# Performance work log

Hardware: AMD Instinct MI355X
Metric: run time of the kernel (lower is better)

## Reference

```python
import jax, jax.numpy as jnp
import numpy as np
from jax import lax

EPS_BN = 1e-5
SMOOTH = 1e-5


def conv3x3(x, w):
    # x: [N,C,H,W], w: [O,I,3,3], stride 1, padding 1 (SAME)
    return lax.conv_general_dilated(
        x, w, window_strides=(1, 1), padding='SAME',
        dimension_numbers=('NCHW', 'OIHW', 'NCHW'))


def batchnorm(x, gamma, beta):
    # training-mode BatchNorm2d: batch statistics over (N,H,W), biased var
    mean = jnp.mean(x, axis=(0, 2, 3), keepdims=True)
    var = jnp.mean(jnp.square(x - mean), axis=(0, 2, 3), keepdims=True)
    g = gamma.reshape(1, -1, 1, 1)
    b = beta.reshape(1, -1, 1, 1)
    return (x - mean) * lax.rsqrt(var + EPS_BN) * g + b


def tanimoto(a, b, axes):
    tpl = jnp.sum(a * b, axis=axes, keepdims=True)
    sq = jnp.sum(a * a + b * b, axis=axes, keepdims=True)
    return (tpl + SMOOTH) / (sq - tpl + SMOOTH)


def tanimoto_compl(a, b, axes):
    return 0.5 * (tanimoto(a, b, axes) + tanimoto(1.0 - a, 1.0 - b, axes))


def setup_inputs() -> dict:
    key = jax.random.key(0)
    ks = jax.random.split(key, 5)
    N, Cin, Cout, H, W = 8, 64, 64, 256, 256
    x = jax.random.normal(ks[0], (N, Cin, H, W), dtype=jnp.float32)
    fan = Cin * 9
    wq = jax.random.normal(ks[1], (Cout, Cin, 3, 3), dtype=jnp.float32) / np.sqrt(fan)
    wk = jax.random.normal(ks[2], (Cout, Cin, 3, 3), dtype=jnp.float32) / np.sqrt(fan)
    wv = jax.random.normal(ks[3], (Cout, Cin, 3, 3), dtype=jnp.float32) / np.sqrt(fan)
    ones = jnp.ones((Cout,), dtype=jnp.float32)
    zeros = jnp.zeros((Cout,), dtype=jnp.float32)
    return {
        'x': x,
        'wq': wq, 'gq': ones, 'bq': zeros,
        'wk': wk, 'gk': ones, 'bk': zeros,
        'wv': wv, 'gv': ones, 'bv': zeros,
        'g_norm': ones, 'b_norm': zeros,
    }


def reference(x, wq, gq, bq, wk, gk, bk, wv, gv, bv, g_norm, b_norm):
    q = jax.nn.sigmoid(batchnorm(conv3x3(x, wq), gq, bq))
    k = jax.nn.sigmoid(batchnorm(conv3x3(x, wk), gk, bk))
    v = jax.nn.sigmoid(batchnorm(conv3x3(x, wv), gv, bv))
    attn_spatial = tanimoto_compl(q, k, axes=(1,))      # [N,1,H,W]
    attn_channel = tanimoto_compl(q, k, axes=(2, 3))    # [N,C,1,1]
    attention = 0.5 * (attn_spatial * v + attn_channel * v)
    return batchnorm(attention, g_norm, b_norm)
```

## Files before the change

### kernel.cpp

```cpp
#include <hip/hip_runtime.h>

typedef unsigned short u16;
typedef __attribute__((ext_vector_type(8))) short short8;
typedef __attribute__((ext_vector_type(4))) float f32x4;
typedef __attribute__((ext_vector_type(16))) float f32x16;

#define OFF_SUMS 0ul
#define OFF_WT   26624ul
#define OFF_ASP  247808ul
#define OFF_CONV 2344960ul
#define S_SUM   0
#define S_SSQ   768
#define M_A1    1920
#define M_A23   2432
#define M_A45   2944
#define M_V1    3456
#define M_V2    3968
#define M_AV    4480
#define M_AV2   4992
#define M_A2V2  5504
#define S_NFLOAT 6656

__device__ __forceinline__ float bf2f(u16 v) {
  union { unsigned u; float f; } x; x.u = ((unsigned)v) << 16; return x.f;
}
__device__ __forceinline__ u16 f2bf(float f) {
  union { float f; unsigned u; } x; x.f = f;
  unsigned r = x.u + 0x7fffu + ((x.u >> 16) & 1u);
  return (u16)(r >> 16);
}
__device__ __forceinline__ float frcp(float x) { return __builtin_amdgcn_rcpf(x); }
__device__ __forceinline__ float sigmoidf_(float x) { return frcp(1.f + __expf(-x)); }

template <int CTRL, int RMASK>
__device__ __forceinline__ float dpp_add(float x) {
  int m = __builtin_amdgcn_update_dpp(0, __builtin_bit_cast(int, x), CTRL, RMASK, 0xf, true);
  return x + __builtin_bit_cast(float, m);
}
__device__ __forceinline__ float wsum64(float x) {
  x = dpp_add<0x111, 0xf>(x);
  x = dpp_add<0x112, 0xf>(x);
  x = dpp_add<0x114, 0xf>(x);
  x = dpp_add<0x118, 0xf>(x);
  x = dpp_add<0x142, 0xa>(x);
  x = dpp_add<0x143, 0xc>(x);
  return __builtin_bit_cast(float, __builtin_amdgcn_readlane(__builtin_bit_cast(int, x), 63));
}

__global__ void tr_k(const float* __restrict__ x, u16* __restrict__ xt,
                     const float* __restrict__ wq, const float* __restrict__ wk,
                     const float* __restrict__ wv, u16* __restrict__ wt) {
  const int bid = blockIdx.x;
  const int tid = threadIdx.x;
  if (bid >= 4096) {
    int i = (bid - 4096) * 256 + tid;
    if (i >= 110592) return;
    int j = i & 7, l = (i >> 3) & 63, kc = (i >> 9) & 3;
    int t2 = i >> 11;
    int ocg = t2 % 6, dydx = t2 / 6;
    int oc = ocg * 32 + (l & 31);
    int ch = kc * 16 + (l >> 5) * 8 + j;
    int cs = oc >> 6, ol = oc & 63;
    const float* src = cs == 0 ? wq : (cs == 1 ? wk : wv);
    wt[i] = f2bf(src[(ol * 64 + ch) * 9 + dydx]);
    return;
  }
  __shared__ u16 t[64][130];
  const int wtile = bid & 1, h = (bid >> 1) & 255, n = bid >> 9;
  const int w0 = wtile << 7;
#pragma unroll
  for (int it = 0; it < 8; ++it) {
    int i = it * 256 + tid;
    int c = i >> 5, w4 = (i & 31) << 2;
    const f32x4 v = *(const f32x4*)(&x[(((long)((n << 6) + c)) << 16) + (h << 8) + w0 + w4]);
    unsigned p0 = (unsigned)f2bf(v[0]) | ((unsigned)f2bf(v[1]) << 16);
    unsigned p1 = (unsigned)f2bf(v[2]) | ((unsigned)f2bf(v[3]) << 16);
    *(unsigned*)(&t[c][w4]) = p0;
    *(unsigned*)(&t[c][w4 + 2]) = p1;
  }
  __syncthreads();
#pragma unroll
  for (int it = 0; it < 4; ++it) {
    int i = it * 256 + tid;
    int c8 = (i & 7) << 3, w = i >> 3;
    unsigned short u[8];
#pragma unroll
    for (int j = 0; j < 8; ++j) u[j] = t[c8 + j][w];
    uint4 val;
    val.x = (unsigned)u[0] | ((unsigned)u[1] << 16);
    val.y = (unsigned)u[2] | ((unsigned)u[3] << 16);
    val.z = (unsigned)u[4] | ((unsigned)u[5] << 16);
    val.w = (unsigned)u[6] | ((unsigned)u[7] << 16);
    *(uint4*)(xt + (long)((((n << 8) + h) << 8) + w0 + w) * 64 + c8) = val;
  }
}

__global__ __launch_bounds__(256, 2) void conv_k(const u16* __restrict__ xt,
                                                 const u16* __restrict__ wt,
                                                 u16* __restrict__ conv,
                                                 float* __restrict__ S) {
  __shared__ u16 lx[3 * 8320];
  const int bid = blockIdx.x;
  const int wtile = bid & 1, h = (bid >> 1) & 255, n = bid >> 9;
  const int w0 = wtile << 7;
  const int tid = threadIdx.x;
  for (int g = tid; g < 3120; g += 256) {
    int row = g / 1040;
    int r2 = g - row * 1040;
    int w = r2 >> 3, cg = r2 & 7;
    int hs = h + row - 1, wsr = w0 + w - 1;
    uint4 val = make_uint4(0u, 0u, 0u, 0u);
    if ((unsigned)hs < 256u && (unsigned)wsr < 256u)
      val = *(const uint4*)(xt + (long)((((n << 8) + hs) << 8) + wsr) * 64 + (cg << 3));
    int idx = ((w << 6) + (cg << 3)) ^ ((w & 7) << 3);
    *(uint4*)(&lx[row * 8320 + idx]) = val;
  }
  __syncthreads();
  const int lane = tid & 63, wave = tid >> 6;
  const int l31 = lane & 31, half = lane >> 5;
  const int wm = wave & 1, wn = wave >> 1;
  f32x16 acc[3][2];
#pragma unroll
  for (int a = 0; a < 3; ++a)
#pragma unroll
    for (int b = 0; b < 2; ++b)
#pragma unroll
      for (int e = 0; e < 16; ++e) acc[a][b][e] = 0.f;

#pragma unroll
  for (int dy = 0; dy < 3; ++dy) {
#pragma unroll
    for (int dx = 0; dx < 3; ++dx) {
      const u16* wp = wt + (dy * 3 + dx) * 12288;
      short8 bfr[3][4];
#pragma unroll
      for (int nt = 0; nt < 3; ++nt)
#pragma unroll
        for (int kc = 0; kc < 4; ++kc)
          bfr[nt][kc] = *(const short8*)(wp + ((wn * 3 + nt) * 4 + kc) * 512 + lane * 8);
#pragma unroll
      for (int kc = 0; kc < 4; ++kc) {
        short8 afr[2];
#pragma unroll
        for (int mt = 0; mt < 2; ++mt) {
          const int px = wm * 64 + mt * 32 + l31 + dx;
          const int chb = kc * 16 + half * 8;
          int idx = ((px << 6) + chb) ^ ((px & 7) << 3);
          afr[mt] = *(const short8*)(&lx[dy * 8320 + idx]);
        }
#pragma unroll
        for (int mt = 0; mt < 2; ++mt)
#pragma unroll
          for (int nt = 0; nt < 3; ++nt)
            acc[nt][mt] = __builtin_amdgcn_mfma_f32_32x32x16_bf16(afr[mt], bfr[nt][kc], acc[nt][mt], 0, 0, 0);
      }
    }
  }
  const long pix0 = (long)bid * 128 + wm * 64;
#pragma unroll
  for (int nt = 0; nt < 3; ++nt) {
    const int oc = wn * 96 + nt * 32 + l31;
#pragma unroll
    for (int mt = 0; mt < 2; ++mt) {
      const long pxb = pix0 + mt * 32 + half * 4;
#pragma unroll
      for (int rq = 0; rq < 4; ++rq)
#pragma unroll
        for (int rr = 0; rr < 4; ++rr) {
          const long px = pxb + rr + 8 * rq;
          conv[px * 192 + oc] = f2bf(acc[nt][mt][rq * 4 + rr]);
        }
    }
  }
  const int sh = (bid & 3) * 192;
#pragma unroll
  for (int nt = 0; nt < 3; ++nt) {
    float s = 0.f, ss = 0.f;
#pragma unroll
    for (int mt = 0; mt < 2; ++mt)
#pragma unroll
      for (int r = 0; r < 16; ++r) {
        float x = acc[nt][mt][r];
        s += x; ss += x * x;
      }
    s += __shfl_xor(s, 32); ss += __shfl_xor(ss, 32);
    if (lane < 32) {
      const int oc = wn * 96 + nt * 32 + lane;
      atomicAdd(&S[S_SUM + sh + oc], s);
      atomicAdd(&S[S_SSQ + sh + oc], ss);
    }
  }
}

__global__ void k3_k(const u16* __restrict__ conv, float* __restrict__ S, float* __restrict__ asp,
                     const float* __restrict__ gq, const float* __restrict__ bq,
                     const float* __restrict__ gk, const float* __restrict__ bk,
                     const float* __restrict__ gv, const float* __restrict__ bv) {
  __shared__ float red[4][8][64];
  __shared__ float scb[192], bib[192];
  const int tid = threadIdx.x, lane = tid & 63, wave = tid >> 6;
  const int bid = blockIdx.x;
  const int n = bid >> 9;
  const long p0 = (long)bid * 128 + wave * 32;
  if (tid < 192) {
    int cv = tid >> 6, c = tid & 63;
    float g = cv == 0 ? gq[c] : (cv == 1 ? gk[c] : gv[c]);
    float b = cv == 0 ? bq[c] : (cv == 1 ? bk[c] : bv[c]);
    float sm = 0.f, sq2 = 0.f;
#pragma unroll
    for (int sh = 0; sh < 4; ++sh) { sm += S[S_SUM + sh * 192 + tid]; sq2 += S[S_SSQ + sh * 192 + tid]; }
    const float inv = 1.f / 524288.f;
    float mean = sm * inv;
    float var = sq2 * inv - mean * mean;
    float rstd = rsqrtf(var + 1e-5f);
    float sc = g * rstd;
    scb[tid] = sc;
    bib[tid] = b - mean * sc;
  }
  __syncthreads();
  const float sq = scb[lane], bq_ = bib[lane];
  const float sk = scb[64 + lane], bk_ = bib[64 + lane];
  const float sv = scb[128 + lane], bv_ = bib[128 + lane];
  float A1 = 0.f, A23 = 0.f, A45 = 0.f, V1 = 0.f, V2 = 0.f, AV = 0.f, AV2 = 0.f, A2V2 = 0.f;
  float myasp = 0.f;
#pragma unroll 4
  for (int i = 0; i < 32; ++i) {
    const u16* row = conv + (p0 + i) * 192;
    float q = sigmoidf_(bf2f(row[lane]) * sq + bq_);
    float k = sigmoidf_(bf2f(row[64 + lane]) * sk + bk_);
    float v = sigmoidf_(bf2f(row[128 + lane]) * sv + bv_);
    float p1 = q * k, p23 = q * q + k * k, p45 = q + k;
    A1 += p1; A23 += p23; A45 += p45;
    float s1 = wsum64(p1);
    float s23 = wsum64(p23);
    float s45 = wsum64(p45);
    const float sm = 1e-5f;
    float t1 = (s1 + sm) * frcp(s23 - s1 + sm);
    float t2 = (64.f - s45 + s1 + sm) * frcp(64.f - s45 + s23 - s1 + sm);
    float a = 0.5f * (t1 + t2);
    if (i == (lane & 31)) myasp = a;
    float av = a * v;
    V1 += v; V2 += v * v; AV += av; AV2 += av * v; A2V2 += av * av;
  }
  if (lane < 32) asp[p0 + lane] = myasp;
  red[wave][0][lane] = A1;  red[wave][1][lane] = A23; red[wave][2][lane] = A45;
  red[wave][3][lane] = V1;  red[wave][4][lane] = V2;  red[wave][5][lane] = AV;
  red[wave][6][lane] = AV2; red[wave][7][lane] = A2V2;
  __syncthreads();
  if (tid < 64) {
    const int mb[8] = {M_A1, M_A23, M_A45, M_V1, M_V2, M_AV, M_AV2, M_A2V2};
#pragma unroll
    for (int m = 0; m < 8; ++m) {
      float t = red[0][m][tid] + red[1][m][tid] + red[2][m][tid] + red[3][m][tid];
      atomicAdd(&S[mb[m] + n * 64 + tid], t);
    }
  }
}

__global__ void k6_k(const u16* __restrict__ conv, const float* __restrict__ S,
                     const float* __restrict__ asp, float* __restrict__ out,
                     const float* __restrict__ gv, const float* __restrict__ bv,
                     const float* __restrict__ gn, const float* __restrict__ bn_) {
  __shared__ float t[128][65];
  __shared__ float svv[64], bvv[64], achb[64], sAv[64], bAv[64];
  const int tid = threadIdx.x, lane = tid & 63, wave = tid >> 6;
  const int n = blockIdx.x >> 9;
  const int hw0 = (blockIdx.x & 511) << 7;
  const long P0 = (long)blockIdx.x * 128;
  if (tid < 64) {
    const float inv = 1.f / 524288.f;
    float sm = 0.f, sq2 = 0.f;
#pragma unroll
    for (int sh = 0; sh < 4; ++sh) {
      sm += S[S_SUM + sh * 192 + 128 + tid];
      sq2 += S[S_SSQ + sh * 192 + 128 + tid];
    }
    float mean = sm * inv;
    float var = sq2 * inv - mean * mean;
    float rstd = rsqrtf(var + 1e-5f);
    float sv = gv[tid] * rstd;
    svv[tid] = sv;
    bvv[tid] = bv[tid] - mean * sv;
    const float smc = 1e-5f, cnt = 65536.f;
    float s1 = 0.f, s2 = 0.f, myach = 0.f;
#pragma unroll
    for (int nn = 0; nn < 8; ++nn) {
      int idx = nn * 64 + tid;
      float A1 = S[M_A1 + idx], A23 = S[M_A23 + idx], A45 = S[M_A45 + idx];
      float t1 = (A1 + smc) / (A23 - A1 + smc);
      float t2 = (cnt - A45 + A1 + smc) / (cnt - A45 + A23 - A1 + smc);
      float ach = 0.5f * (t1 + t2);
      if (nn == n) myach = ach;
      s1 += 0.5f * (S[M_AV + idx] + ach * S[M_V1 + idx]);
      s2 += 0.25f * (S[M_A2V2 + idx] + 2.f * ach * S[M_AV2 + idx] + ach * ach * S[M_V2 + idx]);
    }
    float mean2 = s1 * inv;
    float var2 = s2 * inv - mean2 * mean2;
    float rstd2 = rsqrtf(var2 + 1e-5f);
    float sA = gn[tid] * rstd2;
    sAv[tid] = sA;
    bAv[tid] = bn_[tid] - mean2 * sA;
    achb[tid] = myach;
  }
  __syncthreads();
  const float sv = svv[lane], bvx = bvv[lane];
  const float av = achb[lane];
  const float sA = sAv[lane], bA = bAv[lane];
  for (int i = wave; i < 128; i += 4) {
    const long p = P0 + i;
    float v = sigmoidf_(bf2f(conv[p * 192 + 128 + lane]) * sv + bvx);
    float att = 0.5f * (asp[p] + av) * v;
    t[i][lane] = att * sA + bA;
  }
  __syncthreads();
  const int c = tid >> 2, sub = tid & 3;
  const long plane = ((long)((n << 6) + c)) << 16;
  for (int i = 0; i < 8; ++i) {
    const int pst = (i * 4 + sub) << 2;
    f32x4 vbuf;
#pragma unroll
    for (int j = 0; j < 4; ++j) vbuf[j] = t[pst + j][c];
    *(f32x4*)(&out[plane + hw0 + pst]) = vbuf;
  }
}

extern "C" void kernel_launch(void* const* d_in, const int* in_sizes, int n_in,
                              void* d_out, int out_size, void* d_ws, size_t ws_size,
                              hipStream_t stream) {
  (void)in_sizes; (void)n_in; (void)out_size; (void)ws_size;
  const float* x  = (const float*)d_in[0];
  const float* wq = (const float*)d_in[1];
  const float* gq = (const float*)d_in[2];
  const float* bq = (const float*)d_in[3];
  const float* wk = (const float*)d_in[4];
  const float* gk = (const float*)d_in[5];
  const float* bk = (const float*)d_in[6];
  const float* wv = (const float*)d_in[7];
  const float* gv = (const float*)d_in[8];
  const float* bv = (const float*)d_in[9];
  const float* gn = (const float*)d_in[10];
  const float* bn_ = (const float*)d_in[11];
  char* ws = (char*)d_ws;
  float* S   = (float*)(ws + OFF_SUMS);
  u16* wt    = (u16*)(ws + OFF_WT);
  float* asp = (float*)(ws + OFF_ASP);
  u16* conv  = (u16*)(ws + OFF_CONV);
  float* out = (float*)d_out;
  u16* xt  = (u16*)d_out;

  (void)hipMemsetAsync(S, 0, S_NFLOAT * 4, stream);
  tr_k<<<4528, 256, 0, stream>>>(x, xt, wq, wk, wv, wt);
  conv_k<<<4096, 256, 0, stream>>>(xt, wt, conv, S);
  k3_k<<<4096, 256, 0, stream>>>(conv, S, asp, gq, bq, gk, bk, gv, bv);
  k6_k<<<4096, 256, 0, stream>>>(conv, S, asp, out, gv, bv, gn, bn_);
}
```

Before: 551.2 us.

## Pad and pre-swizzle transposed input so conv tiles load directly into LDS

The transpose kernel now writes a zero-padded 258x258 NHWC bf16 layout with the channel-group XOR swizzle applied in global memory, and extra blocks zero the border. The conv kernel then fills its shared-memory halo rows with contiguous global_load_lds DMA transfers, with no bounds checks, register staging or per-element swizzle. This removes address arithmetic and VGPR round trips from the conv prologue. The cost is slightly larger intermediate writes, extra border-zeroing blocks, and a bit more LDS per block.

Result: no change. 546.3 us (-0.9%).

```diff
diff --git a/kernel.cpp b/kernel.cpp
--- a/kernel.cpp
+++ b/kernel.cpp
@@ -52,8 +52,8 @@
                      const float* __restrict__ wv, u16* __restrict__ wt) {
   const int bid = blockIdx.x;
   const int tid = threadIdx.x;
-  if (bid >= 4096) {
-    int i = (bid - 4096) * 256 + tid;
+  if (bid >= 4104) {
+    int i = (bid - 4104) * 256 + tid;
     if (i >= 110592) return;
     int j = i & 7, l = (i >> 3) & 63, kc = (i >> 9) & 3;
     int t2 = i >> 11;
@@ -65,6 +65,20 @@
     wt[i] = f2bf(src[(ol * 64 + ch) * 9 + dydx]);
     return;
   }
+  if (bid >= 4096) {
+    const int n = bid - 4096;
+    const uint4 z = make_uint4(0u, 0u, 0u, 0u);
+    for (int t = tid; t < 8224; t += 256) {
+      int cell = t >> 3, g = t & 7;
+      int row, col;
+      if (cell < 258) { row = 0; col = cell; }
+      else if (cell < 516) { row = 257; col = cell - 258; }
+      else if (cell < 772) { row = cell - 516 + 1; col = 0; }
+      else { row = cell - 772 + 1; col = 257; }
+      *(uint4*)(xt + ((long)(n * 258 + row) * 258 + col) * 64 + (g << 3)) = z;
+    }
+    return;
+  }
   __shared__ u16 t[64][130];
   const int wtile = bid & 1, h = (bid >> 1) & 255, n = bid >> 9;
   const int w0 = wtile << 7;
@@ -82,7 +96,8 @@
 #pragma unroll
   for (int it = 0; it < 4; ++it) {
     int i = it * 256 + tid;
-    int c8 = (i & 7) << 3, w = i >> 3;
+    int g = i & 7, w = i >> 3;
+    int c8 = g << 3;
     unsigned short u[8];
 #pragma unroll
     for (int j = 0; j < 8; ++j) u[j] = t[c8 + j][w];
@@ -91,7 +106,9 @@
     val.y = (unsigned)u[2] | ((unsigned)u[3] << 16);
     val.z = (unsigned)u[4] | ((unsigned)u[5] << 16);
     val.w = (unsigned)u[6] | ((unsigned)u[7] << 16);
-    *(uint4*)(xt + (long)((((n << 8) + h) << 8) + w0 + w) * 64 + c8) = val;
+    const int pw = w0 + w + 1;
+    const int gs = g ^ (pw & 7);
+    *(uint4*)(xt + ((long)(n * 258 + h + 1) * 258 + pw) * 64 + (gs << 3)) = val;
   }
 }
 
@@ -99,24 +116,25 @@
                                                  const u16* __restrict__ wt,
                                                  u16* __restrict__ conv,
                                                  float* __restrict__ S) {
-  __shared__ u16 lx[3 * 8320];
+  __shared__ u16 lx[3 * 8704];
   const int bid = blockIdx.x;
   const int wtile = bid & 1, h = (bid >> 1) & 255, n = bid >> 9;
   const int w0 = wtile << 7;
   const int tid = threadIdx.x;
-  for (int g = tid; g < 3120; g += 256) {
-    int row = g / 1040;
-    int r2 = g - row * 1040;
-    int w = r2 >> 3, cg = r2 & 7;
-    int hs = h + row - 1, wsr = w0 + w - 1;
-    uint4 val = make_uint4(0u, 0u, 0u, 0u);
-    if ((unsigned)hs < 256u && (unsigned)wsr < 256u)
-      val = *(const uint4*)(xt + (long)((((n << 8) + hs) << 8) + wsr) * 64 + (cg << 3));
-    int idx = ((w << 6) + (cg << 3)) ^ ((w & 7) << 3);
-    *(uint4*)(&lx[row * 8320 + idx]) = val;
-  }
-  __syncthreads();
   const int lane = tid & 63, wave = tid >> 6;
+  {
+    const long rowbase = ((long)(n * 258 + h) * 258 + w0) * 64;
+    for (int c = wave; c < 51; c += 4) {
+      const int s = (c >= 34) ? 2 : (c >= 17 ? 1 : 0);
+      const int lc = c - s * 17;
+      const int loff = s * 8704 + lc * 512 + lane * 8;
+      const long goff = rowbase + (long)s * 16512 + lc * 512 + lane * 8;
+      __builtin_amdgcn_global_load_lds(
+          (const __attribute__((address_space(1))) unsigned int*)(xt + goff),
+          (__attribute__((address_space(3))) unsigned int*)(&lx[loff]), 16, 0, 0);
+    }
+  }
+  __syncthreads();
   const int l31 = lane & 31, half = lane >> 5;
   const int wm = wave & 1, wn = wave >> 1;
   f32x16 acc[3][2];
@@ -146,7 +164,7 @@
           const int px = wm * 64 + mt * 32 + l31 + dx;
           const int chb = kc * 16 + half * 8;
           int idx = ((px << 6) + chb) ^ ((px & 7) << 3);
-          afr[mt] = *(const short8*)(&lx[dy * 8320 + idx]);
+          afr[mt] = *(const short8*)(&lx[dy * 8704 + idx]);
         }
 #pragma unroll
         for (int mt = 0; mt < 2; ++mt)
@@ -349,7 +367,7 @@
   u16* xt  = (u16*)d_out;
 
   (void)hipMemsetAsync(S, 0, S_NFLOAT * 4, stream);
-  tr_k<<<4528, 256, 0, stream>>>(x, xt, wq, wk, wv, wt);
+  tr_k<<<4536, 256, 0, stream>>>(x, xt, wq, wk, wv, wt);
   conv_k<<<4096, 256, 0, stream>>>(xt, wt, conv, S);
   k3_k<<<4096, 256, 0, stream>>>(conv, S, asp, gq, bq, gk, bk, gv, bv);
   k6_k<<<4096, 256, 0, stream>>>(conv, S, asp, out, gv, bv, gn, bn_);
```
